# Kernel optimization log

Hardware: AMD Instinct MI355X
Metric: run time of the kernel (lower is better)

The kernel has to match this reference:

```python
import jax, jax.numpy as jnp
import numpy as np

TAU = 0.25
EPS = 1e-6
H, D = 4, 64  # num_heads, out_channels per head


def kernel_feat(data, proj, is_query):
    # softmax_kernel_transformation (Performer positive random features), sigma=1
    d = data.shape[-1]
    x = data * (float(d) ** -0.25)            # data_normalizer = d^{-1/4}
    ratio = float(proj.shape[0]) ** -0.5      # m^{-1/2}
    dd = jnp.einsum('bnhd,md->bnhm', x, proj)
    diag = 0.5 * jnp.sum(x * x, axis=-1, keepdims=True)
    if is_query:
        mx = jnp.max(dd, axis=-1, keepdims=True)
    else:
        mx = jnp.max(dd, axis=(1, -1), keepdims=True)  # max over M then over N
    return ratio * (jnp.exp(dd - diag - mx) + EPS)


def setup_inputs() -> dict:
    key = jax.random.key(0)
    ks = jax.random.split(key, 12)
    N, E, C = 50000, 800000, 128
    M, K = 30, 10
    z = jax.random.normal(ks[0], (1, N, C), dtype=jnp.float32)
    edge_index = jax.random.randint(ks[1], (2, E), 0, N)
    u = jax.random.uniform(ks[2], (N, 1, H, K), dtype=jnp.float32, minval=1e-8, maxval=1.0)
    gumbels = -jnp.log(-jnp.log(u)) / TAU  # Gumbel(0,1)/tau, matches torch -exp().log()/tau
    proj = jax.random.normal(ks[3], (M, D), dtype=jnp.float32)
    s_in = 1.0 / np.sqrt(C)
    s_o = 1.0 / np.sqrt(H * D)
    return {
        'z': z, 'edge_index': edge_index, 'gumbels': gumbels, 'proj': proj,
        'Wq_w': jax.random.normal(ks[4], (C, H * D), dtype=jnp.float32) * s_in,
        'Wq_b': jnp.zeros((H * D,), dtype=jnp.float32),
        'Wk_w': jax.random.normal(ks[5], (C, H * D), dtype=jnp.float32) * s_in,
        'Wk_b': jnp.zeros((H * D,), dtype=jnp.float32),
        'Wv_w': jax.random.normal(ks[6], (C, H * D), dtype=jnp.float32) * s_in,
        'Wv_b': jnp.zeros((H * D,), dtype=jnp.float32),
        'Wo_w': jax.random.normal(ks[7], (H * D, D), dtype=jnp.float32) * s_o,
        'Wo_b': jnp.zeros((D,), dtype=jnp.float32),
    }


def reference(z, edge_index, gumbels, proj, Wq_w, Wq_b, Wk_w, Wk_b, Wv_w, Wv_b, Wo_w, Wo_b):
    B, N, _ = z.shape
    inv_sqrt_tau = 1.0 / jnp.sqrt(jnp.float32(TAU))
    q = ((z @ Wq_w + Wq_b).reshape(B, N, H, D)) * inv_sqrt_tau
    k = ((z @ Wk_w + Wk_b).reshape(B, N, H, D)) * inv_sqrt_tau
    v = (z @ Wv_w + Wv_b).reshape(B, N, H, D)
    qp = jnp.transpose(kernel_feat(q, proj, True), (1, 0, 2, 3))   # [N,B,H,M]
    kp = jnp.transpose(kernel_feat(k, proj, False), (1, 0, 2, 3))  # [N,B,H,M]
    vp = jnp.transpose(v, (1, 0, 2, 3))                            # [N,B,H,D]
    # Gumbel-perturbed keys: [N,B,H,K,M]
    kg = kp[:, :, :, None, :] * jnp.exp(gumbels)[..., None]
    kvs = jnp.einsum('nbhkm,nbhd->bhkmd', kg, vp)
    z_num = jnp.einsum('nbhm,bhkmd->nbhkd', qp, kvs)               # [N,B,H,K,D]
    z_den = jnp.einsum('nbhm,bhkm->nbhk', qp, kg.sum(axis=0))      # [N,B,H,K]
    z_out = jnp.mean(z_num / z_den[..., None], axis=3)             # [N,B,H,D]
    z_out = jnp.transpose(z_out, (1, 0, 2, 3))                     # [B,N,H,D]
    # edge attention weights for edge loss
    start, end = edge_index[0], edge_index[1]
    num = jnp.einsum('ebhm,ebhm->ebh', qp[end], kp[start])
    den = jnp.einsum('nbhm,bhm->nbh', qp, kp.sum(axis=0))[end]
    A_weight = jnp.transpose(num / den, (1, 0, 2))                 # [B,E,H]
    out = z_out.reshape(B, N, H * D) @ Wo_w + Wo_b                 # [B,N,D]
    return out, A_weight
```

## Files before the change

### kernel.cpp

```cpp
#include <hip/hip_runtime.h>
#include <math.h>

#define NH 4
#define ND 64
#define NC 128
#define NHD 256
#define NM 30
#define NK 10
#define EPSF 1e-6f
#define RATIO 0.18257418583505536f
#define QKSCALE 0.7071067811865476f
#define NSEG 48
#define NSEG2 128

typedef float f32x4 __attribute__((ext_vector_type(4)));
typedef short s16x8 __attribute__((ext_vector_type(8)));

__device__ __forceinline__ unsigned f2ord(float f){ unsigned b=__float_as_uint(f); return (b&0x80000000u)?~b:(b|0x80000000u); }
__device__ __forceinline__ float ord2f(unsigned u){ return __uint_as_float((u&0x80000000u)?(u&0x7fffffffu):~u); }
__device__ __forceinline__ ushort f2bf(float f){ unsigned b=__float_as_uint(f); return (ushort)((b + 0x7fffu + ((b>>16)&1u))>>16); }
__device__ __forceinline__ float bf2f(ushort u){ return __uint_as_float(((unsigned)u)<<16); }
__device__ __forceinline__ void bfsplit(float p, unsigned& hi, unsigned& lo){
    unsigned pb = __float_as_uint(p);
    unsigned t  = pb + 0x8000u;
    unsigned hf = t & 0xffff0000u;
    hi = t >> 16;
    lo = __float_as_uint(p - __uint_as_float(hf)) >> 16;
}

__global__ __launch_bounds__(256) void k_prep(const float* __restrict__ Wq,
    const float* __restrict__ Wk, const float* __restrict__ Wv,
    const float* __restrict__ proj, const float* __restrict__ bq,
    const float* __restrict__ bk, ushort* __restrict__ Wt_h,
    ushort* __restrict__ Wt_l, float* __restrict__ bd, float* __restrict__ kpT,
    ushort* __restrict__ vT16, unsigned* __restrict__ mxk_u,
    int zwork, int N, int Npad)
{
    __shared__ float wd[16*129];
    int b = blockIdx.x;
    int tid = threadIdx.x;
    if (b < 48){
        int idx = b*256 + tid;
        int lane = idx & 63, ks = (idx>>6)&3, tile = idx>>8;
        int c = tile*16 + (lane&15);
        int k0 = ks*32 + (lane>>4)*8;
        const float* W; int cc;
        if (c < 256)      { W = Wq; cc = c; }
        else if (c < 512) { W = Wk; cc = c-256; }
        else              { W = Wv; cc = c-512; }
        #pragma unroll
        for (int j=0;j<8;j++){
            float w = W[(size_t)(k0+j)*NHD + cc];
            ushort h = f2bf(w);
            Wt_h[(size_t)idx*8+j] = h;
            Wt_l[(size_t)idx*8+j] = f2bf(w - bf2f(h));
        }
    } else if (b < 64){
        int dt = b - 48;
        int cl = tid & 15, rc = tid >> 4;
        int cd = dt*16 + cl;
        int isq = (cd < 128);
        int hm = cd & 127;
        int valid = (hm < 120);
        int hh = valid ? hm/30 : 0, m = valid ? hm%30 : 0;
        const float* W = isq ? Wq : Wk;
        const float* prow = proj + (size_t)m*ND;
        #pragma unroll
        for (int rr=0; rr<8; rr++){
            int row = rc*8 + rr;
            float s = 0.f;
            if (valid){
                const float* wr = W + (size_t)row*NHD + hh*64;
                for (int d=0; d<64; d++) s = fmaf(wr[d], prow[d], s);
                s *= QKSCALE;
            }
            wd[cl*129 + row] = s;
        }
        if (tid < 16){
            int cd2 = dt*16 + tid;
            int hm2 = cd2 & 127;
            float s = 0.f;
            if (hm2 < 120){
                int hh2 = hm2/30, m2 = hm2%30;
                const float* bvec = (cd2 < 128) ? bq : bk;
                const float* pr2 = proj + (size_t)m2*ND;
                for (int d=0; d<64; d++) s = fmaf(bvec[hh2*64+d], pr2[d], s);
                s *= QKSCALE;
            }
            bd[cd2] = s;
        }
        __syncthreads();
        int ks = tid >> 6, lane = tid & 63;
        int colL = lane & 15, k0 = ks*32 + (lane>>4)*8;
        unsigned hi[8], lo[8];
        #pragma unroll
        for (int j=0;j<8;j++){
            float v = wd[colL*129 + k0 + j];
            bfsplit(v, hi[j], lo[j]);
        }
        uint4 ph, pl;
        ph.x=hi[0]|(hi[1]<<16); ph.y=hi[2]|(hi[3]<<16); ph.z=hi[4]|(hi[5]<<16); ph.w=hi[6]|(hi[7]<<16);
        pl.x=lo[0]|(lo[1]<<16); pl.y=lo[2]|(lo[3]<<16); pl.z=lo[4]|(lo[5]<<16); pl.w=lo[6]|(lo[7]<<16);
        size_t off = ((size_t)(48+dt)*4 + ks)*64 + lane;
        ((uint4*)Wt_h)[off] = ph;
        ((uint4*)Wt_l)[off] = pl;
    } else {
        int idx = (b-64)*256 + tid;
        int tail = Npad - N;
        int w1 = 8*Npad, w2 = 128*tail, w3 = 256*tail;
        if (idx < w1){
            int r = idx / Npad, c = idx % Npad;
            int hh = r>>1, m = 30 + (r&1);
            kpT[((size_t)(hh*32+m))*Npad + c] = 0.f;
        } else if (idx < w1+w2){
            int j = idx - w1; int r = j / tail, c = N + j % tail;
            kpT[(size_t)r*Npad + c] = 0.f;
        } else if (idx < w1+w2+w3){
            int j = idx - w1 - w2; int r = j / tail, c = N + j % tail;
            vT16[(size_t)r*Npad + c] = 0;
        } else if (idx >= zwork && idx < zwork + 4){
            mxk_u[idx - zwork] = 0u;
        }
    }
}

__global__ __launch_bounds__(256) void k_qkv(
    const float* __restrict__ z,
    const ushort* __restrict__ Wt_h, const ushort* __restrict__ Wt_l,
    const float* __restrict__ bq, const float* __restrict__ bk,
    const float* __restrict__ bv, const float* __restrict__ bd,
    float* __restrict__ qp, ushort* __restrict__ qpe,
    float* __restrict__ dd_k, float* __restrict__ diag_k,
    ushort* __restrict__ vT16, int N, int Npad)
{
    __shared__ float pq[32*132];
    __shared__ float diagq[32*4];
    __shared__ float mxs[32*4];
    int tid = threadIdx.x;
    int n0 = blockIdx.x * 32;
    int w = tid >> 6, lane = tid & 63;
    int l15 = lane & 15, kgrp = lane >> 4;

    s16x8 ah[2][4], al[2][4];
    #pragma unroll
    for (int g=0; g<2; g++){
        int nn = n0 + g*16 + l15; if (nn > N-1) nn = N-1;
        const float* zrow = z + (size_t)nn*NC;
        #pragma unroll
        for (int ks=0;ks<4;ks++){
            f32x4 f0 = *(const f32x4*)(zrow + ks*32 + kgrp*8);
            f32x4 f1 = *(const f32x4*)(zrow + ks*32 + kgrp*8 + 4);
            #pragma unroll
            for (int j=0;j<4;j++){
                float v0 = f0[j]; ushort h0 = f2bf(v0);
                ah[g][ks][j]   = (short)h0; al[g][ks][j]   = (short)f2bf(v0 - bf2f(h0));
                float v1 = f1[j]; ushort h1 = f2bf(v1);
                ah[g][ks][4+j] = (short)h1; al[g][ks][4+j] = (short)f2bf(v1 - bf2f(h1));
            }
        }
    }

    float sq0[4] = {0.f,0.f,0.f,0.f}, sq1[4] = {0.f,0.f,0.f,0.f};
    const uint4* WH = (const uint4*)Wt_h;
    const uint4* WL = (const uint4*)Wt_l;

    for (int nt=0; nt<16; nt++){
        int tile = w*16 + nt;
        f32x4 acc0 = {0.f,0.f,0.f,0.f}, acc1 = {0.f,0.f,0.f,0.f};
        #pragma unroll
        for (int ks=0;ks<4;ks++){
            uint4 bhu = WH[(size_t)(tile*4+ks)*64 + lane];
            uint4 blu = WL[(size_t)(tile*4+ks)*64 + lane];
            s16x8 bh = __builtin_bit_cast(s16x8, bhu);
            s16x8 bl = __builtin_bit_cast(s16x8, blu);
            acc0 = __builtin_amdgcn_mfma_f32_16x16x32_bf16(ah[0][ks], bl, acc0, 0,0,0);
            acc0 = __builtin_amdgcn_mfma_f32_16x16x32_bf16(al[0][ks], bh, acc0, 0,0,0);
            acc0 = __builtin_amdgcn_mfma_f32_16x16x32_bf16(ah[0][ks], bh, acc0, 0,0,0);
            acc1 = __builtin_amdgcn_mfma_f32_16x16x32_bf16(ah[1][ks], bl, acc1, 0,0,0);
            acc1 = __builtin_amdgcn_mfma_f32_16x16x32_bf16(al[1][ks], bh, acc1, 0,0,0);
            acc1 = __builtin_amdgcn_mfma_f32_16x16x32_bf16(ah[1][ks], bh, acc1, 0,0,0);
        }
        int c = tile*16 + l15;
        if (c < 512){
            int ccc = c & 255;
            float bias = (c < 256) ? bq[ccc] : bk[ccc];
            #pragma unroll
            for (int i=0;i<4;i++){
                float x0 = (acc0[i]+bias)*QKSCALE; sq0[i] = fmaf(x0,x0,sq0[i]);
                float x1 = (acc1[i]+bias)*QKSCALE; sq1[i] = fmaf(x1,x1,sq1[i]);
            }
            if ((nt&3)==3){
                int hh = nt>>2;
                #pragma unroll
                for (int i=0;i<4;i++){
                    float s0 = sq0[i], s1 = sq1[i];
                    s0 += __shfl_xor(s0,1); s0 += __shfl_xor(s0,2);
                    s0 += __shfl_xor(s0,4); s0 += __shfl_xor(s0,8);
                    s1 += __shfl_xor(s1,1); s1 += __shfl_xor(s1,2);
                    s1 += __shfl_xor(s1,4); s1 += __shfl_xor(s1,8);
                    if (l15==0){
                        int nd0 = kgrp*4+i, nd1 = 16+kgrp*4+i;
                        if (w==0){ diagq[nd0*4+hh] = 0.5f*s0; diagq[nd1*4+hh] = 0.5f*s1; }
                        else {
                            int na = n0+nd0, nb2 = n0+nd1;
                            if (na < N) diag_k[(size_t)na*4+hh] = 0.5f*s0;
                            if (nb2 < N) diag_k[(size_t)nb2*4+hh] = 0.5f*s1;
                        }
                    }
                    sq0[i]=0.f; sq1[i]=0.f;
                }
            }
        } else if (c < 768){
            int cv = c - 512;
            float bias = bv[cv];
            {
                ushort t0=f2bf(acc0[0]+bias), t1=f2bf(acc0[1]+bias);
                ushort t2=f2bf(acc0[2]+bias), t3=f2bf(acc0[3]+bias);
                int nb = n0 + kgrp*4;
                ushort* dst = &vT16[(size_t)cv*Npad + nb];
                if (nb+4 <= N){ uint2 pk; pk.x=(unsigned)t0|((unsigned)t1<<16); pk.y=(unsigned)t2|((unsigned)t3<<16); *(uint2*)dst=pk; }
                else { if(nb<N)dst[0]=t0; if(nb+1<N)dst[1]=t1; if(nb+2<N)dst[2]=t2; if(nb+3<N)dst[3]=t3; }
            }
            {
                ushort t0=f2bf(acc1[0]+bias), t1=f2bf(acc1[1]+bias);
                ushort t2=f2bf(acc1[2]+bias), t3=f2bf(acc1[3]+bias);
                int nb = n0 + 16 + kgrp*4;
                ushort* dst = &vT16[(size_t)cv*Npad + nb];
                if (nb+4 <= N){ uint2 pk; pk.x=(unsigned)t0|((unsigned)t1<<16); pk.y=(unsigned)t2|((unsigned)t3<<16); *(uint2*)dst=pk; }
                else { if(nb<N)dst[0]=t0; if(nb+1<N)dst[1]=t1; if(nb+2<N)dst[2]=t2; if(nb+3<N)dst[3]=t3; }
            }
        } else {
            int cd = c - 768;
            float bias = bd[cd];
            if (cd < 128){
                #pragma unroll
                for (int i=0;i<4;i++){
                    pq[(kgrp*4+i)*132 + cd]      = acc0[i]+bias;
                    pq[(16+kgrp*4+i)*132 + cd]   = acc1[i]+bias;
                }
            } else {
                int hm = cd - 128;
                if (hm < 120){
                    int hh = hm/30, m = hm%30;
                    size_t base = (size_t)hh*N*NM;
                    #pragma unroll
                    for (int i=0;i<4;i++){
                        int na = n0+kgrp*4+i, nb2 = n0+16+kgrp*4+i;
                        if (na < N)  dd_k[base + (size_t)na*NM + m]  = acc0[i]+bias;
                        if (nb2 < N) dd_k[base + (size_t)nb2*NM + m] = acc1[i]+bias;
                    }
                }
            }
        }
    }
    __syncthreads();

    if (tid < 128){
        int node = tid>>2, hh = tid&3;
        const float* pr = &pq[node*132 + hh*30];
        float mx = -3.0e38f;
        #pragma unroll
        for (int m=0;m<NM;m++) mx = fmaxf(mx, pr[m]);
        mxs[tid] = mx;
    }
    __syncthreads();

    for (int idx = tid; idx < 32*120; idx += 256){
        int node = idx/120, hm = idx%120;
        int n = n0 + node;
        if (n >= N) continue;
        int hh = hm/30;
        float val = RATIO * (__expf(pq[node*132+hm] - diagq[node*4+hh] - mxs[node*4+hh]) + EPSF);
        qp[(size_t)n*120 + hm] = val;
        qpe[(size_t)n*128 + hm] = f2bf(val);
    }
}

__global__ __launch_bounds__(256) void k_maxred(const float* __restrict__ dd_k,
                                                unsigned* __restrict__ mxk_u, int N)
{
    const int CH = 8192;
    int hh = blockIdx.y;
    size_t len = (size_t)N*NM;
    size_t base = (size_t)hh*len;
    size_t lo = (size_t)blockIdx.x*CH;
    size_t hi = lo + CH; if (hi > len) hi = len;
    float m0=-3.0e38f, m1=-3.0e38f, m2=-3.0e38f, m3=-3.0e38f;
    size_t j = lo + (size_t)threadIdx.x*4;
    for (; j + 4 <= hi; j += 1024){
        float4 v = *(const float4*)(dd_k + base + j);
        m0 = fmaxf(m0, v.x); m1 = fmaxf(m1, v.y);
        m2 = fmaxf(m2, v.z); m3 = fmaxf(m3, v.w);
    }
    if (j < hi){
        for (size_t t = j; t < hi; ++t) m0 = fmaxf(m0, dd_k[base + t]);
    }
    float mx = fmaxf(fmaxf(m0, m1), fmaxf(m2, m3));
    for (int o=32;o>0;o>>=1) mx = fmaxf(mx, __shfl_down(mx, o));
    __shared__ float wmax[4];
    if ((threadIdx.x & 63) == 0) wmax[threadIdx.x >> 6] = mx;
    __syncthreads();
    if (threadIdx.x == 0){
        mx = fmaxf(fmaxf(wmax[0],wmax[1]), fmaxf(wmax[2],wmax[3]));
        atomicMax(&mxk_u[hh], f2ord(mx));
    }
}

__global__ __launch_bounds__(256) void k_kp(const float* __restrict__ dd_k,
    const float* __restrict__ diag_k, const unsigned* __restrict__ mxk_u,
    ushort* __restrict__ kpe, float* __restrict__ kpT,
    float* __restrict__ kp_part, int N, int Npad)
{
    __shared__ float tbuf[120*67];
    __shared__ float psum[120];
    int tid = threadIdx.x;
    if (tid < 120) psum[tid] = 0.f;
    float mxk[NH];
    #pragma unroll
    for (int hh=0;hh<NH;hh++) mxk[hh] = ord2f(mxk_u[hh]);
    __syncthreads();
    int n0 = blockIdx.x * 64;
    for (int r = 0; r < 30; r++) {
        int idx = r*256 + tid;
        int nl = idx / 120, hm = idx % 120;
        int n = n0 + nl;
        float val = 0.f;
        if (n < N){
            int hh = hm/30, m = hm%30;
            val = RATIO * (__expf(dd_k[(size_t)hh*N*NM + (size_t)n*NM + m]
                                  - diag_k[(size_t)n*4+hh] - mxk[hh]) + EPSF);
            kpe[(size_t)n*128 + hm] = f2bf(val);
            atomicAdd(&psum[hm], val);
        }
        tbuf[hm*67 + nl] = val;
    }
    __syncthreads();
    for (int i = tid; i < 120*64; i += 256){
        int row = i>>6, cc = i&63;
        int hh = row/30, m = row%30;
        kpT[(size_t)(hh*32+m)*Npad + n0 + cc] = tbuf[row*67 + cc];
    }
    if (tid < 120) kp_part[blockIdx.x*120 + tid] = psum[tid];
}

__global__ __launch_bounds__(256) void k_mid(const float* __restrict__ kp_part,
    float* __restrict__ kp_sum, int nblk,
    const float* __restrict__ gum, float* __restrict__ egT, int N, int Npad)
{
    __shared__ float ws_[4];
    int b = blockIdx.x;
    int tid = threadIdx.x;
    if (b < 120){
        float s = 0.f;
        for (int bb = tid; bb < nblk; bb += 256) s += kp_part[(size_t)bb*120 + b];
        for (int o=32;o>0;o>>=1) s += __shfl_down(s, o);
        if ((tid & 63) == 0) ws_[tid>>6] = s;
        __syncthreads();
        if (tid == 0) kp_sum[b] = ws_[0]+ws_[1]+ws_[2]+ws_[3];
    } else {
        int n0 = (b-120)*64;
        for (int i = tid; i < 64*40; i += 256){
            int nl = i / 40, hk = i % 40;
            int n = n0 + nl;
            if (n >= Npad) continue;
            float v = (n < N) ? __expf(gum[(size_t)n*40 + hk]) : 0.f;
            egT[(size_t)hk*Npad + n] = v;
        }
    }
}

__global__ __launch_bounds__(256,1) void k_kvs2(const float* __restrict__ kpT,
    const float* __restrict__ egT, const ushort* __restrict__ vT16,
    float* __restrict__ part, int Npad)
{
    int seg = blockIdx.x, hh = blockIdx.y;
    int w = threadIdx.x >> 6, lane = threadIdx.x & 63;
    int l15 = lane & 15, lg = lane >> 4;
    int steps_total = Npad/32;
    int per = (steps_total + NSEG-1)/NSEG;
    int s0 = seg*per, s1 = min(steps_total, s0+per);

    const ushort* vbase = vT16 + (size_t)hh*64*Npad;
    const float* kpbase = kpT + (size_t)hh*32*Npad;
    const float* egbase = egT + (size_t)hh*10*Npad;

    f32x4 acc[5][4];
    #pragma unroll
    for (int mt=0;mt<5;mt++)
        #pragma unroll
        for (int nt=0;nt<4;nt++) acc[mt][nt] = (f32x4){0.f,0.f,0.f,0.f};

    for (int st = s0; st < s1; ++st){
        int n0 = st*32 + lg*8;
        s16x8 bf[4];
        #pragma unroll
        for (int nt=0;nt<4;nt++){
            uint4 u = *(const uint4*)(vbase + (size_t)(nt*16 + l15)*Npad + n0);
            bf[nt] = __builtin_bit_cast(s16x8, u);
        }
        #pragma unroll
        for (int mt=0;mt<5;mt++){
            int r = w*80 + mt*16 + l15;
            int m = r & 31, kk = r >> 5;
            const float* kprow = kpbase + (size_t)m*Npad;
            const float* egrow = egbase + (size_t)kk*Npad;
            f32x4 kp0 = *(const f32x4*)(kprow + n0);
            f32x4 kp1 = *(const f32x4*)(kprow + n0 + 4);
            f32x4 eg0 = *(const f32x4*)(egrow + n0);
            f32x4 eg1 = *(const f32x4*)(egrow + n0 + 4);
            f32x4 pr0 = kp0*eg0, pr1 = kp1*eg1;
            unsigned hi[8], lo[8];
            #pragma unroll
            for (int j=0;j<4;j++){
                bfsplit(pr0[j], hi[j], lo[j]);
                bfsplit(pr1[j], hi[4+j], lo[4+j]);
            }
            uint4 ahu, alu;
            ahu.x = hi[0]|(hi[1]<<16); ahu.y = hi[2]|(hi[3]<<16);
            ahu.z = hi[4]|(hi[5]<<16); ahu.w = hi[6]|(hi[7]<<16);
            alu.x = lo[0]|(lo[1]<<16); alu.y = lo[2]|(lo[3]<<16);
            alu.z = lo[4]|(lo[5]<<16); alu.w = lo[6]|(lo[7]<<16);
            s16x8 ah = __builtin_bit_cast(s16x8, ahu);
            s16x8 al = __builtin_bit_cast(s16x8, alu);
            #pragma unroll
            for (int nt=0;nt<4;nt++){
                acc[mt][nt] = __builtin_amdgcn_mfma_f32_16x16x32_bf16(al, bf[nt], acc[mt][nt], 0,0,0);
                acc[mt][nt] = __builtin_amdgcn_mfma_f32_16x16x32_bf16(ah, bf[nt], acc[mt][nt], 0,0,0);
            }
        }
    }
    float* dst = part + ((size_t)hh*NSEG + seg)*20480;
    #pragma unroll
    for (int mt=0;mt<5;mt++)
        #pragma unroll
        for (int nt=0;nt<4;nt++)
            #pragma unroll
            for (int i=0;i<4;i++){
                int rr = w*80 + mt*16 + lg*4 + i;
                dst[rr*64 + nt*16 + l15] = acc[mt][nt][i];
            }
}

__global__ __launch_bounds__(320) void k_kgp(const float* __restrict__ kpT,
    const float* __restrict__ egT, float* __restrict__ kg_part, int Npad)
{
    int s2 = blockIdx.x, hh = blockIdx.y;
    int t = threadIdx.x;
    int kk = t >> 5, m = t & 31;
    int len = Npad / NSEG2;
    int n0 = s2*len;
    float acc = 0.f;
    if (kk < NK && m < NM){
        const f32x4* kr = (const f32x4*)(kpT + ((size_t)(hh*32+m))*Npad + n0);
        const f32x4* er = (const f32x4*)(egT + ((size_t)(hh*10+kk))*Npad + n0);
        for (int i=0;i<len/4;i++){
            f32x4 a = kr[i], b = er[i];
            acc = fmaf(a.x, b.x, acc); acc = fmaf(a.y, b.y, acc);
            acc = fmaf(a.z, b.z, acc); acc = fmaf(a.w, b.w, acc);
        }
    }
    kg_part[((size_t)hh*NSEG2 + s2)*320 + t] = acc;
}

__global__ __launch_bounds__(256) void k_red(const float* __restrict__ part,
    float* __restrict__ kvs, const float* __restrict__ kg_part,
    float* __restrict__ kg_sum)
{
    int b = blockIdx.x, tid = threadIdx.x;
    if (b < 300){
        int o = b*256 + tid;
        if (o >= 76800) return;
        int hh = o / 19200, r = o % 19200;
        int km = r >> 6, d = r & 63;
        int kk = km / 30, m = km % 30;
        size_t base = (size_t)hh*NSEG*20480 + (size_t)(kk*32+m)*64 + d;
        float s = 0.f;
        for (int sg=0; sg<NSEG; sg++) s += part[base + (size_t)sg*20480];
        kvs[o] = s;
    } else {
        int o = (b-300)*256 + tid;
        if (o >= 1200) return;
        int hh = o / 300, r = o % 300;
        int kk = r / 30, m = r % 30;
        float s = 0.f;
        for (int i=0;i<NSEG2;i++) s += kg_part[((size_t)hh*NSEG2 + i)*320 + kk*32 + m];
        kg_sum[o] = s;
    }
}

__global__ __launch_bounds__(256) void k_wkprep(const float* __restrict__ kvs,
    const float* __restrict__ Wo, ushort* __restrict__ WKf_h, ushort* __restrict__ WKf_l)
{
    __shared__ float kv_s[30*65];
    __shared__ float wo_s[64*64];
    __shared__ float wks[32*64];
    int ks = blockIdx.x;
    int h = ks/10, kq = ks%10;
    int tid = threadIdx.x;
    for (int i=tid;i<1920;i+=256){ int m=i>>6, d=i&63; kv_s[m*65+d] = kvs[(size_t)h*19200 + (size_t)(kq*30)*64 + i]; }
    for (int i=tid;i<4096;i+=256) wo_s[i] = Wo[(size_t)h*64*64 + i];
    __syncthreads();
    int m = tid>>3, c0 = (tid&7)*8;
    float acc[8] = {0,0,0,0,0,0,0,0};
    if (m < 30){
        for (int d=0; d<64; d++){
            float kv = kv_s[m*65+d];
            const float* wr = &wo_s[d*64 + c0];
            #pragma unroll
            for (int j=0;j<8;j++) acc[j] = fmaf(kv, wr[j], acc[j]);
        }
    }
    #pragma unroll
    for (int j=0;j<8;j++) wks[m*64 + c0 + j] = acc[j];
    __syncthreads();
    int nt = tid>>6, lane = tid&63, l15 = lane&15, lg = lane>>4;
    unsigned hi[8], lo[8];
    #pragma unroll
    for (int jj=0;jj<8;jj++){
        float v = wks[(lg*8+jj)*64 + nt*16 + l15];
        bfsplit(v, hi[jj], lo[jj]);
    }
    uint4 ph, pl;
    ph.x = hi[0]|(hi[1]<<16); ph.y = hi[2]|(hi[3]<<16); ph.z = hi[4]|(hi[5]<<16); ph.w = hi[6]|(hi[7]<<16);
    pl.x = lo[0]|(lo[1]<<16); pl.y = lo[2]|(lo[3]<<16); pl.z = lo[4]|(lo[5]<<16); pl.w = lo[6]|(lo[7]<<16);
    size_t off = ((size_t)ks*4 + nt)*64 + lane;
    ((uint4*)WKf_h)[off] = ph;
    ((uint4*)WKf_l)[off] = pl;
}

__global__ __launch_bounds__(256) void k_zo(const float* __restrict__ qp,
    const ushort* __restrict__ WKf_h, const ushort* __restrict__ WKf_l,
    const float* __restrict__ kg_sum, const float* __restrict__ kp_sum,
    const float* __restrict__ Wob, ushort* __restrict__ qpe,
    float* __restrict__ out, int N)
{
    __shared__ float kg_s[1200];
    __shared__ float kps_s[120];
    __shared__ uint4 bs[2][2][256];
    int tid = threadIdx.x;
    int w = tid>>6, lane = tid&63, l15 = lane&15, lg = lane>>4;
    int n0 = blockIdx.x*64;
    int n = n0 + w*16 + l15;
    bool nv = (n < N);
    int nc = nv ? n : (N-1);

    for (int i=tid;i<1200;i+=256) kg_s[i] = kg_sum[i];
    if (tid < 120) kps_s[tid] = kp_sum[tid];
    {
        const uint4* sH = (const uint4*)WKf_h;
        const uint4* sL = (const uint4*)WKf_l;
        bs[0][0][tid] = sH[tid];
        bs[0][1][tid] = sL[tid];
    }

    float qA[4][8];
    const float* qrow = qp + (size_t)nc*120;
    #pragma unroll
    for (int h=0;h<4;h++)
      #pragma unroll
      for (int jj=0;jj<8;jj++){
        int m = lg*8+jj;
        qA[h][jj] = (m<30) ? qrow[h*30+m] : 0.f;
      }
    __syncthreads();

    #pragma unroll
    for (int h=0;h<4;h++){
      float p = 0.f;
      #pragma unroll
      for (int jj=0;jj<8;jj++){
        int m = lg*8+jj;
        if (m<30) p = fmaf(qA[h][jj], kps_s[h*30+m], p);
      }
      p += __shfl_xor(p,16);
      p += __shfl_xor(p,32);
      if (lg==0 && nv) ((float*)qpe)[(size_t)n*64 + 60 + h] = p;
    }

    f32x4 acc[4];
    #pragma unroll
    for (int nt=0;nt<4;nt++) acc[nt] = (f32x4){0.f,0.f,0.f,0.f};

    #pragma unroll
    for (int h=0;h<4;h++){
      for (int kq=0;kq<10;kq++){
        int ks = h*10+kq;
        int buf = ks&1;
        if (ks < 39){
            const uint4* sH = (const uint4*)WKf_h + (size_t)(ks+1)*256;
            const uint4* sL = (const uint4*)WKf_l + (size_t)(ks+1)*256;
            bs[buf^1][0][tid] = sH[tid];
            bs[buf^1][1][tid] = sL[tid];
        }
        float p = 0.f;
        #pragma unroll
        for (int jj=0;jj<8;jj++){
          int m = lg*8+jj;
          if (m<30) p = fmaf(qA[h][jj], kg_s[h*300 + kq*30 + m], p);
        }
        p += __shfl_xor(p,16);
        p += __shfl_xor(p,32);
        float sc = 0.1f / p;
        unsigned hi[8], lo[8];
        #pragma unroll
        for (int jj=0;jj<8;jj++) bfsplit(qA[h][jj]*sc, hi[jj], lo[jj]);
        uint4 ahu, alu;
        ahu.x = hi[0]|(hi[1]<<16); ahu.y = hi[2]|(hi[3]<<16);
        ahu.z = hi[4]|(hi[5]<<16); ahu.w = hi[6]|(hi[7]<<16);
        alu.x = lo[0]|(lo[1]<<16); alu.y = lo[2]|(lo[3]<<16);
        alu.z = lo[4]|(lo[5]<<16); alu.w = lo[6]|(lo[7]<<16);
        s16x8 ah = __builtin_bit_cast(s16x8, ahu);
        s16x8 al = __builtin_bit_cast(s16x8, alu);
        #pragma unroll
        for (int nt=0;nt<4;nt++){
            s16x8 bh = __builtin_bit_cast(s16x8, bs[buf][0][nt*64+lane]);
            s16x8 bl = __builtin_bit_cast(s16x8, bs[buf][1][nt*64+lane]);
            acc[nt] = __builtin_amdgcn_mfma_f32_16x16x32_bf16(ah, bl, acc[nt], 0,0,0);
            acc[nt] = __builtin_amdgcn_mfma_f32_16x16x32_bf16(al, bh, acc[nt], 0,0,0);
            acc[nt] = __builtin_amdgcn_mfma_f32_16x16x32_bf16(ah, bh, acc[nt], 0,0,0);
        }
        __syncthreads();
      }
    }

    #pragma unroll
    for (int nt=0;nt<4;nt++){
        float bias = Wob[nt*16 + l15];
        #pragma unroll
        for (int i=0;i<4;i++){
            int node = n0 + w*16 + lg*4 + i;
            if (node < N) out[(size_t)node*64 + nt*16 + l15] = acc[nt][i] + bias;
        }
    }
}

__global__ __launch_bounds__(256) void k_edge(const int* __restrict__ ei,
    const ushort* __restrict__ qpe, const ushort* __restrict__ kpe,
    float* __restrict__ A, int E)
{
    int tid = threadIdx.x;
    int e = blockIdx.x*64 + (tid>>2);
    int sub = tid & 3;
    if (e >= E) return;
    int s = ei[e], t = ei[E + e];
    float dnv = ((const float*)(qpe + (size_t)t*128))[60 + sub];
    const uint4* rq = (const uint4*)(qpe + (size_t)t*128) + sub*4;
    const uint4* rk = (const uint4*)(kpe + (size_t)s*128) + sub*4;
    float numA = 0.f, numB = 0.f;
    int bndw = 15 - sub;
    #define PROC(au,bu,wi) { \
        float a0=__uint_as_float((au)<<16),        b0=__uint_as_float((bu)<<16); \
        float a1=__uint_as_float((au)&0xffff0000u),b1=__uint_as_float((bu)&0xffff0000u); \
        float p = fmaf(a0,b0, a1*b1); \
        if ((wi) < bndw) numA += p; else if (sub < 3) numB += p; }
    #pragma unroll
    for (int j=0;j<4;j++){
        uint4 a = rq[j], b = rk[j];
        PROC(a.x, b.x, j*4+0)
        PROC(a.y, b.y, j*4+1)
        PROC(a.z, b.z, j*4+2)
        PROC(a.w, b.w, j*4+3)
    }
    #undef PROC
    int lane = tid & 63;
    float nbIn = __shfl(numB, (lane > 0) ? (lane-1) : 0);
    float num = numA + ((sub > 0) ? nbIn : 0.f);
    A[(size_t)e*4 + sub] = num / dnv;
}

extern "C" void kernel_launch(void* const* d_in, const int* in_sizes, int n_in,
                              void* d_out, int out_size, void* d_ws, size_t ws_size,
                              hipStream_t stream)
{
    const float* z    = (const float*)d_in[0];
    const int*   ei   = (const int*)d_in[1];
    const float* gum  = (const float*)d_in[2];
    const float* proj = (const float*)d_in[3];
    const float* Wq   = (const float*)d_in[4];
    const float* bq   = (const float*)d_in[5];
    const float* Wk   = (const float*)d_in[6];
    const float* bk   = (const float*)d_in[7];
    const float* Wv   = (const float*)d_in[8];
    const float* bv   = (const float*)d_in[9];
    const float* Wo   = (const float*)d_in[10];
    const float* Wob  = (const float*)d_in[11];
    int N = in_sizes[0] / NC;
    int E = in_sizes[1] / 2;
    int Npad = (N + 511) & ~511;

    float* ws = (float*)d_ws;
    size_t o = 0;
    #define ALIGN64 o = (o + 63) & ~(size_t)63;
    float* qp       = ws + o; o += (size_t)N*120;
    ALIGN64
    float* vbuf     = ws + o; o += (size_t)N*NHD;
    ALIGN64
    float* dd_k     = ws + o; o += (size_t)NH*N*NM;
    float* egT      = dd_k;
    float* kvs_part = dd_k + (size_t)40*Npad;
    ALIGN64
    float* diag_k   = ws + o; o += (size_t)N*4;
    unsigned* mxk_u = (unsigned*)(ws + o); o += 4;
    ALIGN64
    int nkb = (N+63)/64;
    float* kp_part  = ws + o; o += (size_t)nkb*120;
    float* kp_sum   = ws + o; o += 120;
    ALIGN64
    float* kg_part  = ws + o; o += (size_t)NH*NSEG2*320;
    float* kvs      = ws + o; o += 76800;
    float* kg_sum   = ws + o; o += 1200;
    ALIGN64
    ushort* qpe     = (ushort*)(ws + o); o += (size_t)N*64;
    ALIGN64
    ushort* kpe     = (ushort*)(ws + o); o += (size_t)N*64;
    ALIGN64
    ushort* Wt_h    = (ushort*)(ws + o); o += 64*4*64*8/2;
    ALIGN64
    ushort* Wt_l    = (ushort*)(ws + o); o += 64*4*64*8/2;
    ALIGN64
    float* bd       = ws + o; o += 256;
    ALIGN64
    float* kpT      = ws + o; o += (size_t)128*Npad;
    ALIGN64
    ushort* WKf_h   = (ushort*)(ws + o); o += 40*4*64*8/2;
    ALIGN64
    ushort* WKf_l   = (ushort*)(ws + o); o += 40*4*64*8/2;
    ushort* vT16    = (ushort*)vbuf;

    float* out = (float*)d_out;
    float* A   = out + (size_t)N*ND;

    int tail = Npad - N;
    int zwork = 8*Npad + (128+256)*tail;
    int zb = (zwork + 4 + 255)/256;
    k_prep<<<dim3(64 + zb), dim3(256), 0, stream>>>(Wq, Wk, Wv, proj, bq, bk,
                                                    Wt_h, Wt_l, bd, kpT, vT16,
                                                    mxk_u, zwork, N, Npad);
    k_qkv<<<dim3((N+31)/32), dim3(256), 0, stream>>>(z, Wt_h, Wt_l, bq, bk, bv, bd,
                                                     qp, qpe, dd_k, diag_k, vT16, N, Npad);
    {
        size_t len = (size_t)N*NM;
        int mchunks = (int)((len + 8191)/8192);
        k_maxred<<<dim3(mchunks, 4), dim3(256), 0, stream>>>(dd_k, mxk_u, N);
    }
    k_kp<<<dim3(nkb), dim3(256), 0, stream>>>(dd_k, diag_k, mxk_u, kpe, kpT, kp_part, N, Npad);
    k_mid<<<dim3(120 + Npad/64), dim3(256), 0, stream>>>(kp_part, kp_sum, nkb,
                                                         gum, egT, N, Npad);
    k_kvs2<<<dim3(NSEG, NH), dim3(256), 0, stream>>>(kpT, egT, vT16, kvs_part, Npad);
    k_kgp<<<dim3(NSEG2, NH), dim3(320), 0, stream>>>(kpT, egT, kg_part, Npad);
    k_red<<<dim3(305), dim3(256), 0, stream>>>(kvs_part, kvs, kg_part, kg_sum);
    k_wkprep<<<dim3(40), dim3(256), 0, stream>>>(kvs, Wo, WKf_h, WKf_l);
    k_zo<<<dim3((N+63)/64), dim3(256), 0, stream>>>(qp, WKf_h, WKf_l, kg_sum, kp_sum,
                                                    Wob, qpe, out, N);
    k_edge<<<dim3((E+63)/64), dim3(256), 0, stream>>>(ei, qpe, kpe, A, E);
}
```

Before: 440.7 us.

## Merge independent kernels into multi-role launches and move denominator computation earlier

Combines the kvs MFMA partial kernel, the kg partial-sum kernel and a new per-node denominator (qp·kp_sum) computation into one launch that dispatches work by block index. It also merges the z_out projection kernel with the edge-attention kernel, so the edge blocks can overlap with the MFMA-heavy output blocks. Moving the denominator out of k_zo is what makes this merge legal, because the edge pass reads it from qpe. The changes cut launch count and tail idle time, at the cost of mixing heterogeneous block types that share one register/launch_bounds budget (256,1 for mega1).

```diff
diff --git a/kernel.cpp b/kernel.cpp
--- a/kernel.cpp
+++ b/kernel.cpp
@@ -369,97 +369,115 @@
     }
 }
 
-__global__ __launch_bounds__(256,1) void k_kvs2(const float* __restrict__ kpT,
+__global__ __launch_bounds__(256,1) void k_mega1(const float* __restrict__ kpT,
     const float* __restrict__ egT, const ushort* __restrict__ vT16,
-    float* __restrict__ part, int Npad)
-{
-    int seg = blockIdx.x, hh = blockIdx.y;
-    int w = threadIdx.x >> 6, lane = threadIdx.x & 63;
-    int l15 = lane & 15, lg = lane >> 4;
-    int steps_total = Npad/32;
-    int per = (steps_total + NSEG-1)/NSEG;
-    int s0 = seg*per, s1 = min(steps_total, s0+per);
-
-    const ushort* vbase = vT16 + (size_t)hh*64*Npad;
-    const float* kpbase = kpT + (size_t)hh*32*Npad;
-    const float* egbase = egT + (size_t)hh*10*Npad;
-
-    f32x4 acc[5][4];
-    #pragma unroll
-    for (int mt=0;mt<5;mt++)
-        #pragma unroll
-        for (int nt=0;nt<4;nt++) acc[mt][nt] = (f32x4){0.f,0.f,0.f,0.f};
-
-    for (int st = s0; st < s1; ++st){
-        int n0 = st*32 + lg*8;
-        s16x8 bf[4];
-        #pragma unroll
-        for (int nt=0;nt<4;nt++){
-            uint4 u = *(const uint4*)(vbase + (size_t)(nt*16 + l15)*Npad + n0);
-            bf[nt] = __builtin_bit_cast(s16x8, u);
-        }
-        #pragma unroll
-        for (int mt=0;mt<5;mt++){
-            int r = w*80 + mt*16 + l15;
-            int m = r & 31, kk = r >> 5;
-            const float* kprow = kpbase + (size_t)m*Npad;
-            const float* egrow = egbase + (size_t)kk*Npad;
-            f32x4 kp0 = *(const f32x4*)(kprow + n0);
-            f32x4 kp1 = *(const f32x4*)(kprow + n0 + 4);
-            f32x4 eg0 = *(const f32x4*)(egrow + n0);
-            f32x4 eg1 = *(const f32x4*)(egrow + n0 + 4);
-            f32x4 pr0 = kp0*eg0, pr1 = kp1*eg1;
-            unsigned hi[8], lo[8];
-            #pragma unroll
-            for (int j=0;j<4;j++){
-                bfsplit(pr0[j], hi[j], lo[j]);
-                bfsplit(pr1[j], hi[4+j], lo[4+j]);
-            }
-            uint4 ahu, alu;
-            ahu.x = hi[0]|(hi[1]<<16); ahu.y = hi[2]|(hi[3]<<16);
-            ahu.z = hi[4]|(hi[5]<<16); ahu.w = hi[6]|(hi[7]<<16);
-            alu.x = lo[0]|(lo[1]<<16); alu.y = lo[2]|(lo[3]<<16);
-            alu.z = lo[4]|(lo[5]<<16); alu.w = lo[6]|(lo[7]<<16);
-            s16x8 ah = __builtin_bit_cast(s16x8, ahu);
-            s16x8 al = __builtin_bit_cast(s16x8, alu);
+    float* __restrict__ part, float* __restrict__ kg_part,
+    const float* __restrict__ qp, const float* __restrict__ kp_sum,
+    ushort* __restrict__ qpe, int N, int Npad)
+{
+    __shared__ float kps_s[120];
+    int b = blockIdx.x;
+    int tid = threadIdx.x;
+    if (b < 192){
+        int seg = b % NSEG, hh = b / NSEG;
+        int w = tid >> 6, lane = tid & 63;
+        int l15 = lane & 15, lg = lane >> 4;
+        int steps_total = Npad/32;
+        int per = (steps_total + NSEG-1)/NSEG;
+        int s0 = seg*per, s1 = min(steps_total, s0+per);
+
+        const ushort* vbase = vT16 + (size_t)hh*64*Npad;
+        const float* kpbase = kpT + (size_t)hh*32*Npad;
+        const float* egbase = egT + (size_t)hh*10*Npad;
+
+        f32x4 acc[5][4];
+        #pragma unroll
+        for (int mt=0;mt<5;mt++)
+            #pragma unroll
+            for (int nt=0;nt<4;nt++) acc[mt][nt] = (f32x4){0.f,0.f,0.f,0.f};
+
+        for (int st = s0; st < s1; ++st){
+            int n0 = st*32 + lg*8;
+            s16x8 bf[4];
             #pragma unroll
             for (int nt=0;nt<4;nt++){
-                acc[mt][nt] = __builtin_amdgcn_mfma_f32_16x16x32_bf16(al, bf[nt], acc[mt][nt], 0,0,0);
-                acc[mt][nt] = __builtin_amdgcn_mfma_f32_16x16x32_bf16(ah, bf[nt], acc[mt][nt], 0,0,0);
-            }
-        }
-    }
-    float* dst = part + ((size_t)hh*NSEG + seg)*20480;
-    #pragma unroll
-    for (int mt=0;mt<5;mt++)
-        #pragma unroll
-        for (int nt=0;nt<4;nt++)
-            #pragma unroll
-            for (int i=0;i<4;i++){
-                int rr = w*80 + mt*16 + lg*4 + i;
-                dst[rr*64 + nt*16 + l15] = acc[mt][nt][i];
-            }
-}
-
-__global__ __launch_bounds__(320) void k_kgp(const float* __restrict__ kpT,
-    const float* __restrict__ egT, float* __restrict__ kg_part, int Npad)
-{
-    int s2 = blockIdx.x, hh = blockIdx.y;
-    int t = threadIdx.x;
-    int kk = t >> 5, m = t & 31;
-    int len = Npad / NSEG2;
-    int n0 = s2*len;
-    float acc = 0.f;
-    if (kk < NK && m < NM){
-        const f32x4* kr = (const f32x4*)(kpT + ((size_t)(hh*32+m))*Npad + n0);
-        const f32x4* er = (const f32x4*)(egT + ((size_t)(hh*10+kk))*Npad + n0);
-        for (int i=0;i<len/4;i++){
-            f32x4 a = kr[i], b = er[i];
-            acc = fmaf(a.x, b.x, acc); acc = fmaf(a.y, b.y, acc);
-            acc = fmaf(a.z, b.z, acc); acc = fmaf(a.w, b.w, acc);
-        }
-    }
-    kg_part[((size_t)hh*NSEG2 + s2)*320 + t] = acc;
+                uint4 u = *(const uint4*)(vbase + (size_t)(nt*16 + l15)*Npad + n0);
+                bf[nt] = __builtin_bit_cast(s16x8, u);
+            }
+            #pragma unroll
+            for (int mt=0;mt<5;mt++){
+                int r = w*80 + mt*16 + l15;
+                int m = r & 31, kk = r >> 5;
+                const float* kprow = kpbase + (size_t)m*Npad;
+                const float* egrow = egbase + (size_t)kk*Npad;
+                f32x4 kp0 = *(const f32x4*)(kprow + n0);
+                f32x4 kp1 = *(const f32x4*)(kprow + n0 + 4);
+                f32x4 eg0 = *(const f32x4*)(egrow + n0);
+                f32x4 eg1 = *(const f32x4*)(egrow + n0 + 4);
+                f32x4 pr0 = kp0*eg0, pr1 = kp1*eg1;
+                unsigned hi[8], lo[8];
+                #pragma unroll
+                for (int j=0;j<4;j++){
+                    bfsplit(pr0[j], hi[j], lo[j]);
+                    bfsplit(pr1[j], hi[4+j], lo[4+j]);
+                }
+                uint4 ahu, alu;
+                ahu.x = hi[0]|(hi[1]<<16); ahu.y = hi[2]|(hi[3]<<16);
+                ahu.z = hi[4]|(hi[5]<<16); ahu.w = hi[6]|(hi[7]<<16);
+                alu.x = lo[0]|(lo[1]<<16); alu.y = lo[2]|(lo[3]<<16);
+                alu.z = lo[4]|(lo[5]<<16); alu.w = lo[6]|(lo[7]<<16);
+                s16x8 ah = __builtin_bit_cast(s16x8, ahu);
+                s16x8 al = __builtin_bit_cast(s16x8, alu);
+                #pragma unroll
+                for (int nt=0;nt<4;nt++){
+                    acc[mt][nt] = __builtin_amdgcn_mfma_f32_16x16x32_bf16(al, bf[nt], acc[mt][nt], 0,0,0);
+                    acc[mt][nt] = __builtin_amdgcn_mfma_f32_16x16x32_bf16(ah, bf[nt], acc[mt][nt], 0,0,0);
+                }
+            }
+        }
+        float* dst = part + ((size_t)hh*NSEG + seg)*20480;
+        #pragma unroll
+        for (int mt=0;mt<5;mt++)
+            #pragma unroll
+            for (int nt=0;nt<4;nt++)
+                #pragma unroll
+                for (int i=0;i<4;i++){
+                    int rr = w*80 + mt*16 + lg*4 + i;
+                    dst[rr*64 + nt*16 + l15] = acc[mt][nt][i];
+                }
+    } else if (b < 704){
+        int idx = b - 192;
+        int s2 = idx & (NSEG2-1), hh = idx >> 7;
+        int len = Npad / NSEG2;
+        int n0 = s2*len;
+        for (int t = tid; t < 320; t += 256){
+            int kk = t >> 5, m = t & 31;
+            float acc = 0.f;
+            if (kk < NK && m < NM){
+                const f32x4* kr = (const f32x4*)(kpT + ((size_t)(hh*32+m))*Npad + n0);
+                const f32x4* er = (const f32x4*)(egT + ((size_t)(hh*10+kk))*Npad + n0);
+                for (int i=0;i<len/4;i++){
+                    f32x4 a = kr[i], bb = er[i];
+                    acc = fmaf(a.x, bb.x, acc); acc = fmaf(a.y, bb.y, acc);
+                    acc = fmaf(a.z, bb.z, acc); acc = fmaf(a.w, bb.w, acc);
+                }
+            }
+            kg_part[((size_t)hh*NSEG2 + s2)*320 + t] = acc;
+        }
+    } else {
+        int n0 = (b - 704)*64;
+        for (int i=tid;i<120;i+=256) kps_s[i] = kp_sum[i];
+        __syncthreads();
+        int nl = tid >> 2, h = tid & 3;
+        int n = n0 + nl;
+        if (n < N){
+            const float* qrow = qp + (size_t)n*120 + h*30;
+            float p = 0.f;
+            #pragma unroll
+            for (int m=0;m<30;m++) p = fmaf(qrow[m], kps_s[h*30+m], p);
+            ((float*)qpe)[(size_t)n*64 + 60 + h] = p;
+        }
+    }
 }
 
 __global__ __launch_bounds__(256) void k_red(const float* __restrict__ part,
@@ -528,144 +546,127 @@
     ((uint4*)WKf_l)[off] = pl;
 }
 
-__global__ __launch_bounds__(256) void k_zo(const float* __restrict__ qp,
+__global__ __launch_bounds__(256) void k_zoedge(const float* __restrict__ qp,
     const ushort* __restrict__ WKf_h, const ushort* __restrict__ WKf_l,
-    const float* __restrict__ kg_sum, const float* __restrict__ kp_sum,
-    const float* __restrict__ Wob, ushort* __restrict__ qpe,
-    float* __restrict__ out, int N)
+    const float* __restrict__ kg_sum, const float* __restrict__ Wob,
+    const ushort* __restrict__ qpe, const ushort* __restrict__ kpe,
+    const int* __restrict__ ei, float* __restrict__ out, float* __restrict__ A,
+    int zoB, int N, int E)
 {
     __shared__ float kg_s[1200];
-    __shared__ float kps_s[120];
     __shared__ uint4 bs[2][2][256];
     int tid = threadIdx.x;
-    int w = tid>>6, lane = tid&63, l15 = lane&15, lg = lane>>4;
-    int n0 = blockIdx.x*64;
-    int n = n0 + w*16 + l15;
-    bool nv = (n < N);
-    int nc = nv ? n : (N-1);
-
-    for (int i=tid;i<1200;i+=256) kg_s[i] = kg_sum[i];
-    if (tid < 120) kps_s[tid] = kp_sum[tid];
-    {
-        const uint4* sH = (const uint4*)WKf_h;
-        const uint4* sL = (const uint4*)WKf_l;
-        bs[0][0][tid] = sH[tid];
-        bs[0][1][tid] = sL[tid];
-    }
-
-    float qA[4][8];
-    const float* qrow = qp + (size_t)nc*120;
-    #pragma unroll
-    for (int h=0;h<4;h++)
-      #pragma unroll
-      for (int jj=0;jj<8;jj++){
-        int m = lg*8+jj;
-        qA[h][jj] = (m<30) ? qrow[h*30+m] : 0.f;
-      }
-    __syncthreads();
-
-    #pragma unroll
-    for (int h=0;h<4;h++){
-      float p = 0.f;
-      #pragma unroll
-      for (int jj=0;jj<8;jj++){
-        int m = lg*8+jj;
-        if (m<30) p = fmaf(qA[h][jj], kps_s[h*30+m], p);
-      }
-      p += __shfl_xor(p,16);
-      p += __shfl_xor(p,32);
-      if (lg==0 && nv) ((float*)qpe)[(size_t)n*64 + 60 + h] = p;
-    }
-
-    f32x4 acc[4];
-    #pragma unroll
-    for (int nt=0;nt<4;nt++) acc[nt] = (f32x4){0.f,0.f,0.f,0.f};
-
-    #pragma unroll
-    for (int h=0;h<4;h++){
-      for (int kq=0;kq<10;kq++){
-        int ks = h*10+kq;
-        int buf = ks&1;
-        if (ks < 39){
-            const uint4* sH = (const uint4*)WKf_h + (size_t)(ks+1)*256;
-            const uint4* sL = (const uint4*)WKf_l + (size_t)(ks+1)*256;
-            bs[buf^1][0][tid] = sH[tid];
-            bs[buf^1][1][tid] = sL[tid];
-        }
-        float p = 0.f;
-        #pragma unroll
-        for (int jj=0;jj<8;jj++){
-          int m = lg*8+jj;
-          if (m<30) p = fmaf(qA[h][jj], kg_s[h*300 + kq*30 + m], p);
-        }
-        p += __shfl_xor(p,16);
-        p += __shfl_xor(p,32);
-        float sc = 0.1f / p;
-        unsigned hi[8], lo[8];
-        #pragma unroll
-        for (int jj=0;jj<8;jj++) bfsplit(qA[h][jj]*sc, hi[jj], lo[jj]);
-        uint4 ahu, alu;
-        ahu.x = hi[0]|(hi[1]<<16); ahu.y = hi[2]|(hi[3]<<16);
-        ahu.z = hi[4]|(hi[5]<<16); ahu.w = hi[6]|(hi[7]<<16);
-        alu.x = lo[0]|(lo[1]<<16); alu.y = lo[2]|(lo[3]<<16);
-        alu.z = lo[4]|(lo[5]<<16); alu.w = lo[6]|(lo[7]<<16);
-        s16x8 ah = __builtin_bit_cast(s16x8, ahu);
-        s16x8 al = __builtin_bit_cast(s16x8, alu);
+    int b = blockIdx.x;
+    if (b < zoB){
+        int w = tid>>6, lane = tid&63, l15 = lane&15, lg = lane>>4;
+        int n0 = b*64;
+        int n = n0 + w*16 + l15;
+        bool nv = (n < N);
+        int nc = nv ? n : (N-1);
+
+        for (int i=tid;i<1200;i+=256) kg_s[i] = kg_sum[i];
+        {
+            const uint4* sH = (const uint4*)WKf_h;
+            const uint4* sL = (const uint4*)WKf_l;
+            bs[0][0][tid] = sH[tid];
+            bs[0][1][tid] = sL[tid];
+        }
+
+        float qA[4][8];
+        const float* qrow = qp + (size_t)nc*120;
+        #pragma unroll
+        for (int h=0;h<4;h++)
+          #pragma unroll
+          for (int jj=0;jj<8;jj++){
+            int m = lg*8+jj;
+            qA[h][jj] = (m<30) ? qrow[h*30+m] : 0.f;
+          }
+        __syncthreads();
+
+        f32x4 acc[4];
+        #pragma unroll
+        for (int nt=0;nt<4;nt++) acc[nt] = (f32x4){0.f,0.f,0.f,0.f};
+
+        #pragma unroll
+        for (int h=0;h<4;h++){
+          for (int kq=0;kq<10;kq++){
+            int ks = h*10+kq;
+            int buf = ks&1;
+            if (ks < 39){
+                const uint4* sH = (const uint4*)WKf_h + (size_t)(ks+1)*256;
+                const uint4* sL = (const uint4*)WKf_l + (size_t)(ks+1)*256;
+                bs[buf^1][0][tid] = sH[tid];
+                bs[buf^1][1][tid] = sL[tid];
+            }
+            float p = 0.f;
+            #pragma unroll
+            for (int jj=0;jj<8;jj++){
+              int m = lg*8+jj;
+              if (m<30) p = fmaf(qA[h][jj], kg_s[h*300 + kq*30 + m], p);
+            }
+            p += __shfl_xor(p,16);
+            p += __shfl_xor(p,32);
+            float sc = 0.1f / p;
+            unsigned hi[8], lo[8];
+            #pragma unroll
+            for (int jj=0;jj<8;jj++) bfsplit(qA[h][jj]*sc, hi[jj], lo[jj]);
+            uint4 ahu, alu;
+            ahu.x = hi[0]|(hi[1]<<16); ahu.y = hi[2]|(hi[3]<<16);
+            ahu.z = hi[4]|(hi[5]<<16); ahu.w = hi[6]|(hi[7]<<16);
+            alu.x = lo[0]|(lo[1]<<16); alu.y = lo[2]|(lo[3]<<16);
+            alu.z = lo[4]|(lo[5]<<16); alu.w = lo[6]|(lo[7]<<16);
+            s16x8 ah = __builtin_bit_cast(s16x8, ahu);
+            s16x8 al = __builtin_bit_cast(s16x8, alu);
+            #pragma unroll
+            for (int nt=0;nt<4;nt++){
+                s16x8 bh = __builtin_bit_cast(s16x8, bs[buf][0][nt*64+lane]);
+                s16x8 bl = __builtin_bit_cast(s16x8, bs[buf][1][nt*64+lane]);
+                acc[nt] = __builtin_amdgcn_mfma_f32_16x16x32_bf16(ah, bl, acc[nt], 0,0,0);
+                acc[nt] = __builtin_amdgcn_mfma_f32_16x16x32_bf16(al, bh, acc[nt], 0,0,0);
+                acc[nt] = __builtin_amdgcn_mfma_f32_16x16x32_bf16(ah, bh, acc[nt], 0,0,0);
+            }
+            __syncthreads();
+          }
+        }
+
         #pragma unroll
         for (int nt=0;nt<4;nt++){
-            s16x8 bh = __builtin_bit_cast(s16x8, bs[buf][0][nt*64+lane]);
-            s16x8 bl = __builtin_bit_cast(s16x8, bs[buf][1][nt*64+lane]);
-            acc[nt] = __builtin_amdgcn_mfma_f32_16x16x32_bf16(ah, bl, acc[nt], 0,0,0);
-            acc[nt] = __builtin_amdgcn_mfma_f32_16x16x32_bf16(al, bh, acc[nt], 0,0,0);
-            acc[nt] = __builtin_amdgcn_mfma_f32_16x16x32_bf16(ah, bh, acc[nt], 0,0,0);
-        }
-        __syncthreads();
-      }
-    }
-
-    #pragma unroll
-    for (int nt=0;nt<4;nt++){
-        float bias = Wob[nt*16 + l15];
-        #pragma unroll
-        for (int i=0;i<4;i++){
-            int node = n0 + w*16 + lg*4 + i;
-            if (node < N) out[(size_t)node*64 + nt*16 + l15] = acc[nt][i] + bias;
-        }
-    }
-}
-
-__global__ __launch_bounds__(256) void k_edge(const int* __restrict__ ei,
-    const ushort* __restrict__ qpe, const ushort* __restrict__ kpe,
-    float* __restrict__ A, int E)
-{
-    int tid = threadIdx.x;
-    int e = blockIdx.x*64 + (tid>>2);
-    int sub = tid & 3;
-    if (e >= E) return;
-    int s = ei[e], t = ei[E + e];
-    float dnv = ((const float*)(qpe + (size_t)t*128))[60 + sub];
-    const uint4* rq = (const uint4*)(qpe + (size_t)t*128) + sub*4;
-    const uint4* rk = (const uint4*)(kpe + (size_t)s*128) + sub*4;
-    float numA = 0.f, numB = 0.f;
-    int bndw = 15 - sub;
-    #define PROC(au,bu,wi) { \
-        float a0=__uint_as_float((au)<<16),        b0=__uint_as_float((bu)<<16); \
-        float a1=__uint_as_float((au)&0xffff0000u),b1=__uint_as_float((bu)&0xffff0000u); \
-        float p = fmaf(a0,b0, a1*b1); \
-        if ((wi) < bndw) numA += p; else if (sub < 3) numB += p; }
-    #pragma unroll
-    for (int j=0;j<4;j++){
-        uint4 a = rq[j], b = rk[j];
-        PROC(a.x, b.x, j*4+0)
-        PROC(a.y, b.y, j*4+1)
-        PROC(a.z, b.z, j*4+2)
-        PROC(a.w, b.w, j*4+3)
-    }
-    #undef PROC
-    int lane = tid & 63;
-    float nbIn = __shfl(numB, (lane > 0) ? (lane-1) : 0);
-    float num = numA + ((sub > 0) ? nbIn : 0.f);
-    A[(size_t)e*4 + sub] = num / dnv;
+            float bias = Wob[nt*16 + l15];
+            #pragma unroll
+            for (int i=0;i<4;i++){
+                int node = n0 + w*16 + lg*4 + i;
+                if (node < N) out[(size_t)node*64 + nt*16 + l15] = acc[nt][i] + bias;
+            }
+        }
+    } else {
+        int e = (b - zoB)*64 + (tid>>2);
+        int sub = tid & 3;
+        if (e >= E) return;
+        int s = ei[e], t = ei[E + e];
+        float dnv = ((const float*)(qpe + (size_t)t*128))[60 + sub];
+        const uint4* rq = (const uint4*)(qpe + (size_t)t*128) + sub*4;
+        const uint4* rk = (const uint4*)(kpe + (size_t)s*128) + sub*4;
+        float numA = 0.f, numB = 0.f;
+        int bndw = 15 - sub;
+        #define PROC(au,bu,wi) { \
+            float a0=__uint_as_float((au)<<16),        b0=__uint_as_float((bu)<<16); \
+            float a1=__uint_as_float((au)&0xffff0000u),b1=__uint_as_float((bu)&0xffff0000u); \
+            float p = fmaf(a0,b0, a1*b1); \
+            if ((wi) < bndw) numA += p; else if (sub < 3) numB += p; }
+        #pragma unroll
+        for (int j=0;j<4;j++){
+            uint4 a = rq[j], bb = rk[j];
+            PROC(a.x, bb.x, j*4+0)
+            PROC(a.y, bb.y, j*4+1)
+            PROC(a.z, bb.z, j*4+2)
+            PROC(a.w, bb.w, j*4+3)
+        }
+        #undef PROC
+        int lane = tid & 63;
+        float nbIn = __shfl(numB, (lane > 0) ? (lane-1) : 0);
+        float num = numA + ((sub > 0) ? nbIn : 0.f);
+        A[(size_t)e*4 + sub] = num / dnv;
+    }
 }
 
 extern "C" void kernel_launch(void* const* d_in, const int* in_sizes, int n_in,
@@ -746,11 +747,17 @@
     k_kp<<<dim3(nkb), dim3(256), 0, stream>>>(dd_k, diag_k, mxk_u, kpe, kpT, kp_part, N, Npad);
     k_mid<<<dim3(120 + Npad/64), dim3(256), 0, stream>>>(kp_part, kp_sum, nkb,
                                                          gum, egT, N, Npad);
-    k_kvs2<<<dim3(NSEG, NH), dim3(256), 0, stream>>>(kpT, egT, vT16, kvs_part, Npad);
-    k_kgp<<<dim3(NSEG2, NH), dim3(320), 0, stream>>>(kpT, egT, kg_part, Npad);
+    int denb = (N+63)/64;
+    k_mega1<<<dim3(704 + denb), dim3(256), 0, stream>>>(kpT, egT, vT16, kvs_part,
+                                                        kg_part, qp, kp_sum, qpe,
+                                                        N, Npad);
     k_red<<<dim3(305), dim3(256), 0, stream>>>(kvs_part, kvs, kg_part, kg_sum);
     k_wkprep<<<dim3(40), dim3(256), 0, stream>>>(kvs, Wo, WKf_h, WKf_l);
-    k_zo<<<dim3((N+63)/64), dim3(256), 0, stream>>>(qp, WKf_h, WKf_l, kg_sum, kp_sum,
-                                                    Wob, qpe, out, N);
-    k_edge<<<dim3((E+63)/64), dim3(256), 0, stream>>>(ei, qpe, kpe, A, E);
-}
+    {
+        int zoB = (N+63)/64;
+        int edgeB = (E+63)/64;
+        k_zoedge<<<dim3(zoB + edgeB), dim3(256), 0, stream>>>(qp, WKf_h, WKf_l,
+                                                              kg_sum, Wob, qpe, kpe,
+                                                              ei, out, A, zoB, N, E);
+    }
+}
```

New measurement: 405.1 us. 1.09x faster.
